# Kernel tuning notes

Measured on AMD Instinct MI355X. Metric: run time of the kernel, lower is better.

## Reference

```python
import jax, jax.numpy as jnp
import numpy as np

B, C, H, E, V = 64, 200, 1024, 1024, 50257
NEG_INF = -100000.0


def setup_inputs() -> dict:
    key = jax.random.key(0)
    ks = jax.random.split(key, 16)
    p = 1.0 / np.sqrt(H)
    inp = {
        "input": jax.random.normal(ks[0], (B, 1, E), jnp.float32),
        "hidden": jax.random.normal(ks[1], (1, B, H), jnp.float32),
        "list_context_hidden": jax.random.normal(ks[2], (C, B, H), jnp.float32),
        "context_hiddens": jax.random.normal(ks[3], (B, C, H), jnp.float32),
        "topic_vector": jax.random.normal(ks[4], (B, 1, H), jnp.float32),
        "pad_matrix": jax.random.randint(ks[5], (B, C), 0, 2) > 0,
        # attention params
        "dyna_W": jax.random.normal(ks[6], (H, H), jnp.float32) * p,
        "dyna_U": jax.random.normal(ks[7], (H, H), jnp.float32) * p,
        "dyna_v": jax.random.normal(ks[8], (H, 1), jnp.float32) * p,
        # GRU params (torch layout: W_ih (3H, in), W_hh (3H, H))
        "W_ih": jax.random.normal(ks[9], (3 * H, 2 * H + E), jnp.float32) * p,
        "W_hh": jax.random.normal(ks[10], (3 * H, H), jnp.float32) * p,
        "b_ih": jax.random.normal(ks[11], (3 * H,), jnp.float32) * p,
        "b_hh": jax.random.normal(ks[12], (3 * H,), jnp.float32) * p,
        # output projection
        "W_out": jax.random.normal(ks[13], (V, H), jnp.float32) * p,
        "b_out": jax.random.normal(ks[14], (V,), jnp.float32) * p,
    }
    return inp


def _gru_step(x, h, W_ih, W_hh, b_ih, b_hh):
    # x: (B, in), h: (B, H) -> h': (B, H); torch GRUCell math
    gi = x @ W_ih.T + b_ih            # (B, 3H)
    gh = h @ W_hh.T + b_hh            # (B, 3H)
    r = jax.nn.sigmoid(gi[:, :H] + gh[:, :H])
    z = jax.nn.sigmoid(gi[:, H:2 * H] + gh[:, H:2 * H])
    n = jnp.tanh(gi[:, 2 * H:] + r * gh[:, 2 * H:])
    return (1.0 - z) * n + z * h


def reference(input, hidden, list_context_hidden, context_hiddens, topic_vector,
              pad_matrix, dyna_W, dyna_U, dyna_v, W_ih, W_hh, b_ih, b_hh,
              W_out, b_out):
    h0 = hidden[0]                                         # (B, H)
    # additive attention, vectorized over the C contexts
    q = h0 @ dyna_W                                        # (B, H)
    k = jnp.einsum('cbh,hk->cbk', list_context_hidden, dyna_U)  # (C, B, H)
    scores = jnp.tanh(q[None, :, :] + k) @ dyna_v          # (C, B, 1)
    scores = scores[..., 0].T                              # (B, C)
    scores = jnp.where(pad_matrix, NEG_INF, scores)
    attn = jax.nn.softmax(scores, axis=1)                  # (B, C)
    applied = jnp.einsum('bc,bch->bh', attn, context_hiddens)  # (B, H)
    # GRU over a single step
    x = jnp.concatenate([input[:, 0], topic_vector[:, 0], applied], axis=1)  # (B, E+2H)
    h_new = _gru_step(x, h0, W_ih, W_hh, b_ih, b_hh)       # (B, H)
    logits = h_new @ W_out.T + b_out                       # (B, V)
    out = jax.nn.log_softmax(logits, axis=1)
    return out, h_new[None]
```

## Files before the change

kernel.cpp:

```cpp
#include <hip/hip_runtime.h>
#include <hip/hip_bf16.h>
#include <math.h>

constexpr int Bsz = 64, Cctx = 200, Hdim = 1024, Vv = 50257;
constexpr float NEG_INF_V = -100000.0f;

typedef __attribute__((ext_vector_type(8))) short s16x8;
typedef __attribute__((ext_vector_type(4))) float fx4;
typedef unsigned int u32;

__device__ __forceinline__ unsigned short f2bf(float f) {
  unsigned int u = __builtin_bit_cast(unsigned int, f);
  unsigned int r = (u + 0x7fffu + ((u >> 16) & 1u)) >> 16;
  return (unsigned short)r;
}

__device__ __forceinline__ float fast_tanh(float x) {
  float e2 = __expf(2.f * x);
  return 1.f - 2.f / (e2 + 1.f);
}

__device__ __forceinline__ void gl_lds16(const unsigned short* g, unsigned short* l) {
  __builtin_amdgcn_global_load_lds(
      (const __attribute__((address_space(1))) u32*)g,
      (__attribute__((address_space(3))) u32*)l, 16, 0, 0);
}

__global__ __launch_bounds__(256)
void gemm_att(const unsigned short* __restrict__ Ab, const unsigned short* __restrict__ Bb,
              const float* __restrict__ qmat, const float* __restrict__ vvec,
              float* __restrict__ part_sc) {
  __shared__ unsigned short As[2][128 * 64];
  __shared__ unsigned short Bs[2][128 * 64];
  int f = blockIdx.x + blockIdx.y * 8;
  int xcd = f & 7, jj = f >> 3;
  int my = xcd + 8 * (jj % 13), mx = jj / 13;
  if (my >= 100) return;
  const int bm0 = my * 128, bn0 = mx * 128;
  const int tid = threadIdx.x, lane = tid & 63, wid = tid >> 6;
  const int wm0 = (wid >> 1) * 64, wn0 = (wid & 1) * 64;
  const int ar = lane & 15, q4 = lane >> 4;
  const int sw = ar & 7;

  auto STAGE = [&](int buf, int kt) {
    #pragma unroll
    for (int i = 0; i < 4; ++i) {
      int s = tid + i * 256;
      int row = s >> 3;
      int sc = ((s & 7) ^ (row & 7)) * 8;
      gl_lds16(&Ab[(size_t)(bm0 + row) * Hdim + kt + sc], &As[buf][s * 8]);
    }
    #pragma unroll
    for (int i = 0; i < 4; ++i) {
      int s = tid + i * 256;
      int row = s >> 3;
      int sc = ((s & 7) ^ (row & 7)) * 8;
      gl_lds16(&Bb[(size_t)(bn0 + row) * Hdim + kt + sc], &Bs[buf][s * 8]);
    }
  };

  fx4 acc[4][4] = {};
  STAGE(0, 0);
  __syncthreads();
  int buf = 0;

  for (int t = 0; t < 16; ++t) {
    if (t < 15) STAGE(buf ^ 1, (t + 1) * 64);
    asm volatile("" ::: "memory");
    #pragma unroll
    for (int kk = 0; kk < 2; ++kk) {
      s16x8 a[4], b[4];
      #pragma unroll
      for (int i = 0; i < 4; ++i)
        a[i] = *reinterpret_cast<const s16x8*>(
            &As[buf][(wm0 + i * 16 + ar) * 64 + (((kk * 4 + q4) ^ sw) * 8)]);
      #pragma unroll
      for (int j2 = 0; j2 < 4; ++j2)
        b[j2] = *reinterpret_cast<const s16x8*>(
            &Bs[buf][(wn0 + j2 * 16 + ar) * 64 + (((kk * 4 + q4) ^ sw) * 8)]);
      #pragma unroll
      for (int i = 0; i < 4; ++i)
        #pragma unroll
        for (int j2 = 0; j2 < 4; ++j2)
          acc[i][j2] = __builtin_amdgcn_mfma_f32_16x16x32_bf16(a[i], b[j2], acc[i][j2], 0, 0, 0);
    }
    __syncthreads();
    buf ^= 1;
  }

  const int rg = q4 * 4, cg = ar;
  #pragma unroll
  for (int i = 0; i < 4; ++i) {
    #pragma unroll
    for (int p = 0; p < 4; ++p) {
      int mg = bm0 + wm0 + i * 16 + rg + p;
      int brow = mg & 63;
      float rs = 0.f;
      #pragma unroll
      for (int j2 = 0; j2 < 4; ++j2) {
        int ng = bn0 + wn0 + j2 * 16 + cg;
        float t = fast_tanh(acc[i][j2][p] + qmat[brow * Hdim + ng]);
        rs += t * vvec[ng];
      }
      rs += __shfl_xor(rs, 1); rs += __shfl_xor(rs, 2);
      rs += __shfl_xor(rs, 4); rs += __shfl_xor(rs, 8);
      if (cg == 0) part_sc[mx * 12800 + brow * Cctx + (mg >> 6)] = rs;
    }
  }
}

__device__ __forceinline__ void stream_body(const unsigned short* ap, const float* bp,
                                            int K, fx4 acc[4]) {
  float4 b0 = *reinterpret_cast<const float4*>(bp);
  float4 b1 = *reinterpret_cast<const float4*>(bp + 4);
  float4 b2 = *reinterpret_cast<const float4*>(bp + 32);
  float4 b3 = *reinterpret_cast<const float4*>(bp + 36);
  for (int kt = 0; kt < K; kt += 64) {
    float4 c0 = b0, c1 = b1, c2 = b2, c3 = b3;
    if (kt + 64 < K) {
      b0 = *reinterpret_cast<const float4*>(bp + kt + 64);
      b1 = *reinterpret_cast<const float4*>(bp + kt + 68);
      b2 = *reinterpret_cast<const float4*>(bp + kt + 96);
      b3 = *reinterpret_cast<const float4*>(bp + kt + 100);
    }
    s16x8 bf0, bf1;
    bf0[0] = (short)f2bf(c0.x); bf0[1] = (short)f2bf(c0.y);
    bf0[2] = (short)f2bf(c0.z); bf0[3] = (short)f2bf(c0.w);
    bf0[4] = (short)f2bf(c1.x); bf0[5] = (short)f2bf(c1.y);
    bf0[6] = (short)f2bf(c1.z); bf0[7] = (short)f2bf(c1.w);
    bf1[0] = (short)f2bf(c2.x); bf1[1] = (short)f2bf(c2.y);
    bf1[2] = (short)f2bf(c2.z); bf1[3] = (short)f2bf(c2.w);
    bf1[4] = (short)f2bf(c3.x); bf1[5] = (short)f2bf(c3.y);
    bf1[6] = (short)f2bf(c3.z); bf1[7] = (short)f2bf(c3.w);
    #pragma unroll
    for (int i = 0; i < 4; ++i) {
      s16x8 af = *reinterpret_cast<const s16x8*>(ap + (size_t)i * 16 * K + kt);
      acc[i] = __builtin_amdgcn_mfma_f32_16x16x32_bf16(af, bf0, acc[i], 0, 0, 0);
    }
    #pragma unroll
    for (int i = 0; i < 4; ++i) {
      s16x8 af = *reinterpret_cast<const s16x8*>(ap + (size_t)i * 16 * K + kt + 32);
      acc[i] = __builtin_amdgcn_mfma_f32_16x16x32_bf16(af, bf1, acc[i], 0, 0, 0);
    }
  }
}

template<int EPI>
__global__ __launch_bounds__(64)
void stream_gemm(const unsigned short* __restrict__ Ab,
                 const float* __restrict__ Bm, int N, int K,
                 const float* __restrict__ bias, float* __restrict__ Cout) {
  const int lane = threadIdx.x;
  const int n0 = blockIdx.x * 16;
  const int c = lane & 15, qq = lane >> 4;
  const int brow = min(n0 + c, N - 1);
  fx4 acc[4] = {};
  stream_body(Ab + (size_t)c * K + qq * 8, Bm + (size_t)brow * K + qq * 8, K, acc);
  const int n = n0 + c;
  if (n < N) {
    float bv = (EPI == 2) ? bias[n] : 0.f;
    #pragma unroll
    for (int i = 0; i < 4; ++i)
      #pragma unroll
      for (int p = 0; p < 4; ++p)
        Cout[(size_t)(i * 16 + qq * 4 + p) * N + n] = acc[i][p] + bv;
  }
}

__global__ __launch_bounds__(64)
void qgh_gemm(const unsigned short* __restrict__ h0b, const float* __restrict__ Wt,
              const float* __restrict__ Whh, const float* __restrict__ bhh,
              float* __restrict__ q, float* __restrict__ gh) {
  const int lane = threadIdx.x;
  const int gw = blockIdx.x;
  const bool isq = gw < 64;
  const int n0 = isq ? gw * 16 : (gw - 64) * 16;
  const int N = isq ? 1024 : 3072;
  const float* B = isq ? Wt : Whh;
  const int c = lane & 15, qq = lane >> 4;
  fx4 acc[4] = {};
  stream_body(h0b + (size_t)c * 1024 + qq * 8, B + (size_t)(n0 + c) * 1024 + qq * 8, 1024, acc);
  const int n = n0 + c;
  float bv = isq ? 0.f : bhh[n];
  float* C = isq ? q : gh;
  #pragma unroll
  for (int i = 0; i < 4; ++i)
    #pragma unroll
    for (int p = 0; p < 4; ++p)
      C[(size_t)(i * 16 + qq * 4 + p) * N + n] = acc[i][p] + bv;
}

__global__ __launch_bounds__(64)
void gi_split(const unsigned short* __restrict__ xb, const float* __restrict__ Wih,
              float* __restrict__ part) {
  const int lane = threadIdx.x;
  const int t = blockIdx.x;
  const int w = blockIdx.y;
  const int c = lane & 15, qq = lane >> 4;
  constexpr int K = 3072, CH = 768;
  const float* bp = Wih + (size_t)(t * 16 + c) * K + w * CH + qq * 8;
  const unsigned short* ap = xb + (size_t)c * K + w * CH + qq * 8;
  fx4 acc[4] = {};
  float4 b0 = *reinterpret_cast<const float4*>(bp);
  float4 b1 = *reinterpret_cast<const float4*>(bp + 4);
  float4 b2 = *reinterpret_cast<const float4*>(bp + 32);
  float4 b3 = *reinterpret_cast<const float4*>(bp + 36);
  for (int kt = 0; kt < CH; kt += 64) {
    float4 c0 = b0, c1 = b1, c2 = b2, c3 = b3;
    if (kt + 64 < CH) {
      b0 = *reinterpret_cast<const float4*>(bp + kt + 64);
      b1 = *reinterpret_cast<const float4*>(bp + kt + 68);
      b2 = *reinterpret_cast<const float4*>(bp + kt + 96);
      b3 = *reinterpret_cast<const float4*>(bp + kt + 100);
    }
    s16x8 bf0, bf1;
    bf0[0] = (short)f2bf(c0.x); bf0[1] = (short)f2bf(c0.y);
    bf0[2] = (short)f2bf(c0.z); bf0[3] = (short)f2bf(c0.w);
    bf0[4] = (short)f2bf(c1.x); bf0[5] = (short)f2bf(c1.y);
    bf0[6] = (short)f2bf(c1.z); bf0[7] = (short)f2bf(c1.w);
    bf1[0] = (short)f2bf(c2.x); bf1[1] = (short)f2bf(c2.y);
    bf1[2] = (short)f2bf(c2.z); bf1[3] = (short)f2bf(c2.w);
    bf1[4] = (short)f2bf(c3.x); bf1[5] = (short)f2bf(c3.y);
    bf1[6] = (short)f2bf(c3.z); bf1[7] = (short)f2bf(c3.w);
    #pragma unroll
    for (int i = 0; i < 4; ++i) {
      s16x8 af = *reinterpret_cast<const s16x8*>(ap + (size_t)i * 16 * K + kt);
      acc[i] = __builtin_amdgcn_mfma_f32_16x16x32_bf16(af, bf0, acc[i], 0, 0, 0);
    }
    #pragma unroll
    for (int i = 0; i < 4; ++i) {
      s16x8 af = *reinterpret_cast<const s16x8*>(ap + (size_t)i * 16 * K + kt + 32);
      acc[i] = __builtin_amdgcn_mfma_f32_16x16x32_bf16(af, bf1, acc[i], 0, 0, 0);
    }
  }
  float* po = part + (size_t)w * 64 * 3072;
  const int n = t * 16 + c;
  #pragma unroll
  for (int i = 0; i < 4; ++i)
    #pragma unroll
    for (int p = 0; p < 4; ++p)
      po[(size_t)(i * 16 + qq * 4 + p) * 3072 + n] = acc[i][p];
}

__global__ __launch_bounds__(256)
void prep(const float* __restrict__ dW, const float* __restrict__ dU,
          const float* __restrict__ h0, float* __restrict__ Wt,
          unsigned short* __restrict__ ub, unsigned short* __restrict__ h0b) {
  const int z = blockIdx.z;
  const int tx = threadIdx.x & 31, ty = threadIdx.x >> 5;
  if (z < 2) {
    __shared__ float t[32][33];
    const float* in = z ? dU : dW;
    int bx = blockIdx.x * 32, by = blockIdx.y * 32;
    #pragma unroll
    for (int r = 0; r < 32; r += 8) t[ty + r][tx] = in[(size_t)(by + ty + r) * 1024 + bx + tx];
    __syncthreads();
    if (z == 0) {
      #pragma unroll
      for (int r = 0; r < 32; r += 8) Wt[(size_t)(bx + ty + r) * 1024 + by + tx] = t[tx][ty + r];
    } else {
      #pragma unroll
      for (int r = 0; r < 32; r += 8) ub[(size_t)(bx + ty + r) * 1024 + by + tx] = f2bf(t[tx][ty + r]);
    }
  } else {
    if (blockIdx.y) return;
    size_t i = (size_t)(blockIdx.x * 256 + threadIdx.x) * 8;
    float4 a = *reinterpret_cast<const float4*>(h0 + i);
    float4 b = *reinterpret_cast<const float4*>(h0 + i + 4);
    s16x8 h;
    h[0] = (short)f2bf(a.x); h[1] = (short)f2bf(a.y); h[2] = (short)f2bf(a.z); h[3] = (short)f2bf(a.w);
    h[4] = (short)f2bf(b.x); h[5] = (short)f2bf(b.y); h[6] = (short)f2bf(b.z); h[7] = (short)f2bf(b.w);
    *reinterpret_cast<s16x8*>(h0b + i) = h;
  }
}

__global__ void conv_bf16(const float* __restrict__ in, unsigned short* __restrict__ out) {
  size_t i = (size_t)(blockIdx.x * 256 + threadIdx.x) * 8;
  float4 a = *reinterpret_cast<const float4*>(in + i);
  float4 b = *reinterpret_cast<const float4*>(in + i + 4);
  s16x8 h;
  h[0] = (short)f2bf(a.x); h[1] = (short)f2bf(a.y); h[2] = (short)f2bf(a.z); h[3] = (short)f2bf(a.w);
  h[4] = (short)f2bf(b.x); h[5] = (short)f2bf(b.y); h[6] = (short)f2bf(b.z); h[7] = (short)f2bf(b.w);
  *reinterpret_cast<s16x8*>(out + i) = h;
}

__global__ __launch_bounds__(256)
void softmax_applied(const float* __restrict__ part_sc, const int* __restrict__ pad,
                     const float* __restrict__ ch, float* __restrict__ part) {
  const int g = blockIdx.x, b = blockIdx.y, t = threadIdx.x;
  const int lane = t & 63, w = t >> 6;
  __shared__ float at[256];
  __shared__ float red[8];
  float sv = 0.f, v = -3.4e38f;
  if (t < Cctx) {
    float s8 = 0.f;
    #pragma unroll
    for (int mx = 0; mx < 8; ++mx) s8 += part_sc[mx * 12800 + b * Cctx + t];
    sv = pad[b * Cctx + t] ? NEG_INF_V : s8;
    v = sv;
  }
  #pragma unroll
  for (int o = 1; o < 64; o <<= 1) v = fmaxf(v, __shfl_xor(v, o));
  if (lane == 0) red[w] = v;
  __syncthreads();
  float m = fmaxf(fmaxf(red[0], red[1]), fmaxf(red[2], red[3]));
  float e = (t < Cctx) ? expf(sv - m) : 0.f;
  float s = e;
  #pragma unroll
  for (int o = 1; o < 64; o <<= 1) s += __shfl_xor(s, o);
  if (lane == 0) red[4 + w] = s;
  __syncthreads();
  float tot = red[4] + red[5] + red[6] + red[7];
  at[t] = e / tot;
  __syncthreads();
  const int h = t * 4;
  float4 a4 = make_float4(0.f, 0.f, 0.f, 0.f);
  for (int c2 = g * 25; c2 < g * 25 + 25; ++c2) {
    float a = at[c2];
    float4 vv = *reinterpret_cast<const float4*>(&ch[((size_t)b * Cctx + c2) * Hdim + h]);
    a4.x += a * vv.x; a4.y += a * vv.y; a4.z += a * vv.z; a4.w += a * vv.w;
  }
  *reinterpret_cast<float4*>(&part[((size_t)b * 8 + g) * Hdim + h]) = a4;
}

__global__ void build_xb(const float* __restrict__ inp, const float* __restrict__ topic,
                         const float* __restrict__ part, unsigned short* __restrict__ xb) {
  int j = blockIdx.x * 256 + threadIdx.x;
  int b = blockIdx.y;
  float v;
  if (j < 1024) v = inp[b * 1024 + j];
  else if (j < 2048) v = topic[b * 1024 + (j - 1024)];
  else {
    const float* pp = &part[(size_t)b * 8 * Hdim + (j - 2048)];
    v = 0.f;
    #pragma unroll
    for (int g = 0; g < 8; ++g) v += pp[g * Hdim];
  }
  xb[(size_t)b * 3072 + j] = f2bf(v);
}

__global__ void gru_gate(const float* __restrict__ pgi, const float* __restrict__ bih,
                         const float* __restrict__ gh, const float* __restrict__ h0,
                         float* __restrict__ out_h, unsigned short* __restrict__ hnb) {
  int idx = blockIdx.x * 256 + threadIdx.x;
  int b = idx >> 10, j = idx & 1023;
  float gr = bih[j], gz = bih[1024 + j], gn = bih[2048 + j];
  const float* pb = pgi + (size_t)b * 3072;
  #pragma unroll
  for (int w = 0; w < 4; ++w) {
    const float* pw = pb + (size_t)w * 64 * 3072;
    gr += pw[j]; gz += pw[1024 + j]; gn += pw[2048 + j];
  }
  const float* ghb = gh + (size_t)b * 3072;
  float r = 1.f / (1.f + expf(-(gr + ghb[j])));
  float z = 1.f / (1.f + expf(-(gz + ghb[1024 + j])));
  float n = tanhf(gn + r * ghb[2048 + j]);
  float h = (1.f - z) * n + z * h0[idx];
  out_h[idx] = h;
  hnb[idx] = f2bf(h);
}

__global__ __launch_bounds__(1024)
void lse_fused(float* __restrict__ out) {
  const int b = blockIdx.x, t = threadIdx.x, lane = t & 63, w = t >> 6;
  __shared__ float red[16];
  float* row = out + (size_t)b * Vv;
  float m = -3.4e38f;
  for (int i = t; i < Vv; i += 1024) m = fmaxf(m, row[i]);
  #pragma unroll
  for (int o = 1; o < 64; o <<= 1) m = fmaxf(m, __shfl_xor(m, o));
  if (lane == 0) red[w] = m;
  __syncthreads();
  float mm = red[0];
  #pragma unroll
  for (int k = 1; k < 16; ++k) mm = fmaxf(mm, red[k]);
  float s = 0.f;
  for (int i = t; i < Vv; i += 1024) s += expf(row[i] - mm);
  #pragma unroll
  for (int o = 1; o < 64; o <<= 1) s += __shfl_xor(s, o);
  __syncthreads();
  if (lane == 0) red[w] = s;
  __syncthreads();
  float ss = 0.f;
  #pragma unroll
  for (int k = 0; k < 16; ++k) ss += red[k];
  float lse = mm + logf(ss);
  for (int i = t; i < Vv; i += 1024) row[i] -= lse;
}

extern "C" void kernel_launch(void* const* d_in, const int* in_sizes, int n_in,
                              void* d_out, int out_size, void* d_ws, size_t ws_size,
                              hipStream_t stream) {
  const float* input  = (const float*)d_in[0];
  const float* hidden = (const float*)d_in[1];
  const float* lch    = (const float*)d_in[2];
  const float* ch     = (const float*)d_in[3];
  const float* topic  = (const float*)d_in[4];
  const int*   pad    = (const int*)d_in[5];
  const float* dyna_W = (const float*)d_in[6];
  const float* dyna_U = (const float*)d_in[7];
  const float* dyna_v = (const float*)d_in[8];
  const float* W_ih   = (const float*)d_in[9];
  const float* W_hh   = (const float*)d_in[10];
  const float* b_ih   = (const float*)d_in[11];
  const float* b_hh   = (const float*)d_in[12];
  const float* W_out  = (const float*)d_in[13];
  const float* b_out  = (const float*)d_in[14];

  float* out   = (float*)d_out;
  float* out_h = out + (size_t)Bsz * Vv;

  float* p = (float*)d_ws;
  float* Wt      = p; p += 1024 * 1024;
  float* q       = p; p += Bsz * Hdim;
  float* part_sc = p; p += 8 * Bsz * Cctx;
  float* part_ap = p; p += Bsz * 8 * Hdim;
  float* gh      = p; p += Bsz * 3072;
  float* part_gi = p; p += 4 * Bsz * 3072;
  unsigned short* up = (unsigned short*)p;
  unsigned short* ub  = up; up += 1024 * 1024;
  unsigned short* lb  = up; up += (size_t)Cctx * Bsz * Hdim;
  unsigned short* h0b = up; up += Bsz * Hdim;
  unsigned short* hnb = up; up += Bsz * Hdim;
  unsigned short* xb  = up; up += Bsz * 3072;

  prep<<<dim3(32, 32, 3), 256, 0, stream>>>(dyna_W, dyna_U, hidden, Wt, ub, h0b);
  conv_bf16<<<(Cctx * Bsz * Hdim) / 2048, 256, 0, stream>>>(lch, lb);

  qgh_gemm<<<256, 64, 0, stream>>>(h0b, Wt, W_hh, b_hh, q, gh);

  gemm_att<<<dim3(8, 104), 256, 0, stream>>>(lb, ub, q, dyna_v, part_sc);

  softmax_applied<<<dim3(8, Bsz), 256, 0, stream>>>(part_sc, pad, ch, part_ap);
  build_xb<<<dim3(12, Bsz), 256, 0, stream>>>(input, topic, part_ap, xb);

  gi_split<<<dim3(192, 4), 64, 0, stream>>>(xb, W_ih, part_gi);

  gru_gate<<<(Bsz * Hdim) / 256, 256, 0, stream>>>(part_gi, b_ih, gh, hidden, out_h, hnb);

  stream_gemm<2><<<(Vv + 15) / 16, 64, 0, stream>>>(hnb, W_out, Vv, Hdim, b_out, out);

  lse_fused<<<Bsz, 1024, 0, stream>>>(out);
}
```

Baseline: 238.1 us.

## Split log-softmax across blocks per row and deepen weight prefetch

Replaces the one-block-per-row log-softmax with a partial max/sum kernel over 8 chunks per row and a separate wide subtract kernel, so many more blocks cover the 64 rows. The streaming GEMM body now prefetches weights two K-steps ahead, and gi_split reuses that shared body. This costs an extra launch, an extra pass reading the logits, and more registers for the prefetch buffers.

```diff
diff --git a/kernel.cpp b/kernel.cpp
--- a/kernel.cpp
+++ b/kernel.cpp
@@ -110,18 +110,23 @@
 }
 
 __device__ __forceinline__ void stream_body(const unsigned short* ap, const float* bp,
-                                            int K, fx4 acc[4]) {
+                                            int stride, int extent, fx4 acc[4]) {
   float4 b0 = *reinterpret_cast<const float4*>(bp);
   float4 b1 = *reinterpret_cast<const float4*>(bp + 4);
   float4 b2 = *reinterpret_cast<const float4*>(bp + 32);
   float4 b3 = *reinterpret_cast<const float4*>(bp + 36);
-  for (int kt = 0; kt < K; kt += 64) {
+  float4 n0 = *reinterpret_cast<const float4*>(bp + 64);
+  float4 n1 = *reinterpret_cast<const float4*>(bp + 68);
+  float4 n2 = *reinterpret_cast<const float4*>(bp + 96);
+  float4 n3 = *reinterpret_cast<const float4*>(bp + 100);
+  for (int kt = 0; kt < extent; kt += 64) {
     float4 c0 = b0, c1 = b1, c2 = b2, c3 = b3;
-    if (kt + 64 < K) {
-      b0 = *reinterpret_cast<const float4*>(bp + kt + 64);
-      b1 = *reinterpret_cast<const float4*>(bp + kt + 68);
-      b2 = *reinterpret_cast<const float4*>(bp + kt + 96);
-      b3 = *reinterpret_cast<const float4*>(bp + kt + 100);
+    b0 = n0; b1 = n1; b2 = n2; b3 = n3;
+    if (kt + 128 < extent) {
+      n0 = *reinterpret_cast<const float4*>(bp + kt + 128);
+      n1 = *reinterpret_cast<const float4*>(bp + kt + 132);
+      n2 = *reinterpret_cast<const float4*>(bp + kt + 160);
+      n3 = *reinterpret_cast<const float4*>(bp + kt + 164);
     }
     s16x8 bf0, bf1;
     bf0[0] = (short)f2bf(c0.x); bf0[1] = (short)f2bf(c0.y);
@@ -134,12 +139,12 @@
     bf1[6] = (short)f2bf(c3.z); bf1[7] = (short)f2bf(c3.w);
     #pragma unroll
     for (int i = 0; i < 4; ++i) {
-      s16x8 af = *reinterpret_cast<const s16x8*>(ap + (size_t)i * 16 * K + kt);
+      s16x8 af = *reinterpret_cast<const s16x8*>(ap + (size_t)i * 16 * stride + kt);
       acc[i] = __builtin_amdgcn_mfma_f32_16x16x32_bf16(af, bf0, acc[i], 0, 0, 0);
     }
     #pragma unroll
     for (int i = 0; i < 4; ++i) {
-      s16x8 af = *reinterpret_cast<const s16x8*>(ap + (size_t)i * 16 * K + kt + 32);
+      s16x8 af = *reinterpret_cast<const s16x8*>(ap + (size_t)i * 16 * stride + kt + 32);
       acc[i] = __builtin_amdgcn_mfma_f32_16x16x32_bf16(af, bf1, acc[i], 0, 0, 0);
     }
   }
@@ -155,7 +160,7 @@
   const int c = lane & 15, qq = lane >> 4;
   const int brow = min(n0 + c, N - 1);
   fx4 acc[4] = {};
-  stream_body(Ab + (size_t)c * K + qq * 8, Bm + (size_t)brow * K + qq * 8, K, acc);
+  stream_body(Ab + (size_t)c * K + qq * 8, Bm + (size_t)brow * K + qq * 8, K, K, acc);
   const int n = n0 + c;
   if (n < N) {
     float bv = (EPI == 2) ? bias[n] : 0.f;
@@ -179,7 +184,8 @@
   const float* B = isq ? Wt : Whh;
   const int c = lane & 15, qq = lane >> 4;
   fx4 acc[4] = {};
-  stream_body(h0b + (size_t)c * 1024 + qq * 8, B + (size_t)(n0 + c) * 1024 + qq * 8, 1024, acc);
+  stream_body(h0b + (size_t)c * 1024 + qq * 8, B + (size_t)(n0 + c) * 1024 + qq * 8,
+              1024, 1024, acc);
   const int n = n0 + c;
   float bv = isq ? 0.f : bhh[n];
   float* C = isq ? q : gh;
@@ -198,41 +204,9 @@
   const int w = blockIdx.y;
   const int c = lane & 15, qq = lane >> 4;
   constexpr int K = 3072, CH = 768;
-  const float* bp = Wih + (size_t)(t * 16 + c) * K + w * CH + qq * 8;
-  const unsigned short* ap = xb + (size_t)c * K + w * CH + qq * 8;
   fx4 acc[4] = {};
-  float4 b0 = *reinterpret_cast<const float4*>(bp);
-  float4 b1 = *reinterpret_cast<const float4*>(bp + 4);
-  float4 b2 = *reinterpret_cast<const float4*>(bp + 32);
-  float4 b3 = *reinterpret_cast<const float4*>(bp + 36);
-  for (int kt = 0; kt < CH; kt += 64) {
-    float4 c0 = b0, c1 = b1, c2 = b2, c3 = b3;
-    if (kt + 64 < CH) {
-      b0 = *reinterpret_cast<const float4*>(bp + kt + 64);
-      b1 = *reinterpret_cast<const float4*>(bp + kt + 68);
-      b2 = *reinterpret_cast<const float4*>(bp + kt + 96);
-      b3 = *reinterpret_cast<const float4*>(bp + kt + 100);
-    }
-    s16x8 bf0, bf1;
-    bf0[0] = (short)f2bf(c0.x); bf0[1] = (short)f2bf(c0.y);
-    bf0[2] = (short)f2bf(c0.z); bf0[3] = (short)f2bf(c0.w);
-    bf0[4] = (short)f2bf(c1.x); bf0[5] = (short)f2bf(c1.y);
-    bf0[6] = (short)f2bf(c1.z); bf0[7] = (short)f2bf(c1.w);
-    bf1[0] = (short)f2bf(c2.x); bf1[1] = (short)f2bf(c2.y);
-    bf1[2] = (short)f2bf(c2.z); bf1[3] = (short)f2bf(c2.w);
-    bf1[4] = (short)f2bf(c3.x); bf1[5] = (short)f2bf(c3.y);
-    bf1[6] = (short)f2bf(c3.z); bf1[7] = (short)f2bf(c3.w);
-    #pragma unroll
-    for (int i = 0; i < 4; ++i) {
-      s16x8 af = *reinterpret_cast<const s16x8*>(ap + (size_t)i * 16 * K + kt);
-      acc[i] = __builtin_amdgcn_mfma_f32_16x16x32_bf16(af, bf0, acc[i], 0, 0, 0);
-    }
-    #pragma unroll
-    for (int i = 0; i < 4; ++i) {
-      s16x8 af = *reinterpret_cast<const s16x8*>(ap + (size_t)i * 16 * K + kt + 32);
-      acc[i] = __builtin_amdgcn_mfma_f32_16x16x32_bf16(af, bf1, acc[i], 0, 0, 0);
-    }
-  }
+  stream_body(xb + (size_t)c * K + w * CH + qq * 8,
+              Wih + (size_t)(t * 16 + c) * K + w * CH + qq * 8, K, CH, acc);
   float* po = part + (size_t)w * 64 * 3072;
   const int n = t * 16 + c;
   #pragma unroll
@@ -360,32 +334,44 @@
   hnb[idx] = f2bf(h);
 }
 
-__global__ __launch_bounds__(1024)
-void lse_fused(float* __restrict__ out) {
-  const int b = blockIdx.x, t = threadIdx.x, lane = t & 63, w = t >> 6;
-  __shared__ float red[16];
-  float* row = out + (size_t)b * Vv;
+__global__ __launch_bounds__(256)
+void lse_part(const float* __restrict__ out, float* __restrict__ pm, float* __restrict__ ps) {
+  const int g = blockIdx.x, b = blockIdx.y, t = threadIdx.x;
+  const int lane = t & 63, w = t >> 6;
+  __shared__ float red[8];
+  const float* row = out + (size_t)b * Vv;
   float m = -3.4e38f;
-  for (int i = t; i < Vv; i += 1024) m = fmaxf(m, row[i]);
+  for (int i = g * 256 + t; i < Vv; i += 2048) m = fmaxf(m, row[i]);
   #pragma unroll
   for (int o = 1; o < 64; o <<= 1) m = fmaxf(m, __shfl_xor(m, o));
   if (lane == 0) red[w] = m;
   __syncthreads();
-  float mm = red[0];
-  #pragma unroll
-  for (int k = 1; k < 16; ++k) mm = fmaxf(mm, red[k]);
+  float mm = fmaxf(fmaxf(red[0], red[1]), fmaxf(red[2], red[3]));
   float s = 0.f;
-  for (int i = t; i < Vv; i += 1024) s += expf(row[i] - mm);
+  for (int i = g * 256 + t; i < Vv; i += 2048) s += __expf(row[i] - mm);
   #pragma unroll
   for (int o = 1; o < 64; o <<= 1) s += __shfl_xor(s, o);
-  __syncthreads();
-  if (lane == 0) red[w] = s;
-  __syncthreads();
-  float ss = 0.f;
-  #pragma unroll
-  for (int k = 0; k < 16; ++k) ss += red[k];
-  float lse = mm + logf(ss);
-  for (int i = t; i < Vv; i += 1024) row[i] -= lse;
+  if (lane == 0) red[4 + w] = s;
+  __syncthreads();
+  if (t == 0) {
+    pm[b * 8 + g] = mm;
+    ps[b * 8 + g] = red[4] + red[5] + red[6] + red[7];
+  }
+}
+
+__global__ __launch_bounds__(256)
+void lse_sub(float* __restrict__ out, const float* __restrict__ pm,
+             const float* __restrict__ ps) {
+  const int b = blockIdx.y;
+  float M = -3.4e38f;
+  #pragma unroll
+  for (int g = 0; g < 8; ++g) M = fmaxf(M, pm[b * 8 + g]);
+  float S = 0.f;
+  #pragma unroll
+  for (int g = 0; g < 8; ++g) S += ps[b * 8 + g] * __expf(pm[b * 8 + g] - M);
+  float lse = M + logf(S);
+  int i = blockIdx.x * 256 + threadIdx.x;
+  if (i < Vv) out[(size_t)b * Vv + i] -= lse;
 }
 
 extern "C" void kernel_launch(void* const* d_in, const int* in_sizes, int n_in,
@@ -417,6 +403,8 @@
   float* part_ap = p; p += Bsz * 8 * Hdim;
   float* gh      = p; p += Bsz * 3072;
   float* part_gi = p; p += 4 * Bsz * 3072;
+  float* pm      = p; p += Bsz * 8;
+  float* ps      = p; p += Bsz * 8;
   unsigned short* up = (unsigned short*)p;
   unsigned short* ub  = up; up += 1024 * 1024;
   unsigned short* lb  = up; up += (size_t)Cctx * Bsz * Hdim;
@@ -440,5 +428,6 @@
 
   stream_gemm<2><<<(Vv + 15) / 16, 64, 0, stream>>>(hnb, W_out, Vv, Hdim, b_out, out);
 
-  lse_fused<<<Bsz, 1024, 0, stream>>>(out);
-}
+  lse_part<<<dim3(8, Bsz), 256, 0, stream>>>(out, pm, ps);
+  lse_sub<<<dim3((Vv + 255) / 256, Bsz), 256, 0, stream>>>(out, pm, ps);
+}
```

Result: slower. 273.1 us (+14.7%).
